# Kernel tuning notes

Measured on AMD Instinct MI355X. Metric: run time of the kernel, lower is better.

The kernel has to match this reference:

```python
import jax, jax.numpy as jnp
import numpy as np
from jax import lax

D_MODEL = 12
D_STATE = 16
D_CONV = 4
D_INNER = 24
DT_RANK = 4
BN_EPS = 1e-5


def _bn(h, gamma, beta, mean, var):
    # inference-mode BatchNorm2d over channel dim (axis=1)
    inv = gamma / jnp.sqrt(var + BN_EPS)
    return h * inv[None, :, None, None] + (beta - mean * inv)[None, :, None, None]


def _mamba(seq, in_proj_w, conv1d_w, conv1d_b, x_proj_w, dt_proj_w, dt_proj_b, A_log, Dp, out_proj_w):
    # seq: (b, L, d_model)
    b, L, _ = seq.shape
    xz = jnp.einsum('bld,ed->ble', seq, in_proj_w)            # (b, L, 2*d_inner)
    u, res = xz[..., :D_INNER], xz[..., D_INNER:]
    # causal depthwise conv1d
    uc = lax.conv_general_dilated(
        u.transpose(0, 2, 1), conv1d_w,                       # (b,d_inner,L), (d_inner,1,d_conv)
        window_strides=(1,), padding=[(D_CONV - 1, 0)],
        feature_group_count=D_INNER,
        dimension_numbers=('NCH', 'OIH', 'NCH'))
    uc = jax.nn.silu((uc + conv1d_b[None, :, None]).transpose(0, 2, 1))  # (b,L,d_inner)
    x_dbl = jnp.einsum('bld,ed->ble', uc, x_proj_w)           # (b,L,dt_rank+2*d_state)
    delta = jax.nn.softplus(
        jnp.einsum('blr,dr->bld', x_dbl[..., :DT_RANK], dt_proj_w) + dt_proj_b)
    Bm = x_dbl[..., DT_RANK:DT_RANK + D_STATE]                # (b,L,n)
    Cm = x_dbl[..., DT_RANK + D_STATE:]                       # (b,L,n)
    A = -jnp.exp(A_log)                                       # (d_inner, n)
    deltaA = jnp.exp(delta[..., None] * A)                    # (b,L,d,n)
    deltaBu = delta[..., None] * Bm[:, :, None, :] * uc[..., None]

    def step(h, inp):
        dA, dBu, c = inp                                      # (b,d,n),(b,d,n),(b,n)
        h = dA * h + dBu
        y = jnp.einsum('bdn,bn->bd', h, c)
        return h, y

    h0 = jnp.zeros((b, D_INNER, D_STATE), seq.dtype)
    _, ys = lax.scan(step, h0, (deltaA.transpose(1, 0, 2, 3),
                                deltaBu.transpose(1, 0, 2, 3),
                                Cm.transpose(1, 0, 2)))
    y = ys.transpose(1, 0, 2) + uc * Dp                       # (b,L,d_inner)
    y = y * jax.nn.silu(res)
    return jnp.einsum('bld,ed->ble', y, out_proj_w)           # (b,L,d_model)


def setup_inputs() -> dict:
    key = jax.random.key(0)
    ks = jax.random.split(key, 16)
    C_IN, C_MID, L = 256, 512, 16384
    d = dict(
        x=jax.random.normal(ks[0], (1, C_IN, L, D_MODEL), jnp.float32),
        conv1_w=jax.random.normal(ks[1], (C_MID, C_IN), jnp.float32) * 0.05,
        conv1_b=jnp.zeros((C_MID,), jnp.float32),
        bn1_gamma=jnp.ones((C_MID,), jnp.float32),
        bn1_beta=jnp.zeros((C_MID,), jnp.float32),
        bn1_mean=jnp.zeros((C_MID,), jnp.float32),
        bn1_var=jnp.ones((C_MID,), jnp.float32),
        conv2_w=jax.random.normal(ks[2], (1, C_MID), jnp.float32) * 0.05,
        conv2_b=jnp.zeros((1,), jnp.float32),
        bn2_gamma=jnp.ones((1,), jnp.float32),
        bn2_beta=jnp.zeros((1,), jnp.float32),
        bn2_mean=jnp.zeros((1,), jnp.float32),
        bn2_var=jnp.ones((1,), jnp.float32),
        in_proj_w=jax.random.normal(ks[3], (2 * D_INNER, D_MODEL), jnp.float32) * 0.2,
        conv1d_w=jax.random.normal(ks[4], (D_INNER, 1, D_CONV), jnp.float32) * 0.3,
        conv1d_b=jnp.zeros((D_INNER,), jnp.float32),
        x_proj_w=jax.random.normal(ks[5], (DT_RANK + 2 * D_STATE, D_INNER), jnp.float32) * 0.2,
        dt_proj_w=jax.random.normal(ks[6], (D_INNER, DT_RANK), jnp.float32) * 0.2,
        dt_proj_b=jax.random.normal(ks[7], (D_INNER,), jnp.float32) * 0.1 - 4.0,
        A_log=jnp.log(jnp.tile(jnp.arange(1, D_STATE + 1, dtype=jnp.float32), (D_INNER, 1))),
        D=jnp.ones((D_INNER,), jnp.float32),
        out_proj_w=jax.random.normal(ks[8], (D_MODEL, D_INNER), jnp.float32) * 0.2,
        lin_w=jax.random.normal(ks[9], (1, D_MODEL), jnp.float32) * 0.3,
        lin_b=jnp.zeros((1,), jnp.float32),
    )
    return d


def reference(x, conv1_w, conv1_b, bn1_gamma, bn1_beta, bn1_mean, bn1_var,
              conv2_w, conv2_b, bn2_gamma, bn2_beta, bn2_mean, bn2_var,
              in_proj_w, conv1d_w, conv1d_b, x_proj_w, dt_proj_w, dt_proj_b,
              A_log, D, out_proj_w, lin_w, lin_b):
    # 1x1 conv stem + BN + ReLU (x2)
    h = jnp.einsum('bchw,oc->bohw', x, conv1_w) + conv1_b[None, :, None, None]
    h = jax.nn.relu(_bn(h, bn1_gamma, bn1_beta, bn1_mean, bn1_var))
    h = jnp.einsum('bchw,oc->bohw', h, conv2_w) + conv2_b[None, :, None, None]
    h = jax.nn.relu(_bn(h, bn2_gamma, bn2_beta, bn2_mean, bn2_var))  # (1,1,L,12)
    seq = h[0]                                                        # squeeze(0) -> (1, L, 12)
    out = _mamba(seq, in_proj_w, conv1d_w, conv1d_b, x_proj_w,
                 dt_proj_w, dt_proj_b, A_log, D, out_proj_w)
    pred = out[:, -1, :] @ lin_w.T + lin_b                            # (1, 1)
    return pred
```

## Files before the change

kernel.cpp:

```cpp
#include <hip/hip_runtime.h>
#include <math.h>

#define L_SEQ 16384
#define DM    12
#define CIN   256
#define CMID  512
#define NPOS  (L_SEQ * DM)
#define DIN   24
#define DST   16

#define OFF_W1T   0u
#define OFF_B1P   131072u
#define OFF_W2P   131584u
#define OFF_MISC  132096u
#define OFF_SEQ   132112u
#define OFF_DELTA 328720u
#define OFF_G     721936u
#define OFF_BW    1115152u
#define OFF_S     1377296u
#define OFF_LAST  1770512u
#define OFF_HL    1770576u
#define WS_FLOATS_NEEDED (OFF_HL + DIN * DST)

__global__ void k0_prep(const float* __restrict__ W1, const float* __restrict__ b1,
                        const float* __restrict__ g1, const float* __restrict__ be1,
                        const float* __restrict__ m1, const float* __restrict__ v1,
                        const float* __restrict__ w2, const float* __restrict__ b2,
                        const float* __restrict__ g2, const float* __restrict__ be2,
                        const float* __restrict__ m2, const float* __restrict__ v2,
                        float* __restrict__ ws) {
    const int o = blockIdx.x;
    const int c = threadIdx.x;
    const float inv1 = g1[o] * rsqrtf(v1[o] + 1e-5f);
    ws[OFF_W1T + (unsigned)c * CMID + o] = W1[o * CIN + c] * inv1;
    if (c == 0) {
        ws[OFF_B1P + o] = b1[o] * inv1 + be1[o] - m1[o] * inv1;
        const float inv2 = g2[0] * rsqrtf(v2[0] + 1e-5f);
        ws[OFF_W2P + o] = w2[o] * inv2;
        if (o == 0) ws[OFF_MISC] = b2[0] * inv2 + be2[0] - m2[0] * inv2;
    }
}

__launch_bounds__(256, 2)
__global__ void k1_gemm(const float* __restrict__ x, const float* __restrict__ wsr,
                        float* __restrict__ seq) {
    __shared__ float Xl[CIN * 64];
    const int tid  = threadIdx.x;
    const int lane = tid & 63;
    const int wv   = __builtin_amdgcn_readfirstlane(tid >> 6);
    const long p0  = (long)blockIdx.x * 64;

    #pragma unroll
    for (int it = 0; it < 16; ++it) {
        const int idx = it * 256 + tid;
        const int row = idx >> 4;
        const int c4  = (idx & 15) << 2;
        *(float4*)&Xl[row * 64 + c4] =
            *(const float4*)&x[(long)row * NPOS + p0 + c4];
    }
    __syncthreads();

    const float* __restrict__ W1T = wsr + OFF_W1T;
    const float* __restrict__ b1p = wsr + OFF_B1P;
    const float* __restrict__ w2p = wsr + OFF_W2P;

    float sp = 0.f;
    for (int ch = 0; ch < 16; ++ch) {
        const int o0 = ch * 32 + wv * 8;
        float acc[8];
        #pragma unroll
        for (int j = 0; j < 8; ++j) acc[j] = 0.f;
        const float* wb = W1T + o0;
        #pragma unroll 4
        for (int c = 0; c < CIN; ++c) {
            const float xv = Xl[c * 64 + lane];
            const float* wr = wb + c * CMID;
            #pragma unroll
            for (int j = 0; j < 8; ++j) acc[j] = fmaf(wr[j], xv, acc[j]);
        }
        #pragma unroll
        for (int j = 0; j < 8; ++j) {
            float h = acc[j] + b1p[o0 + j];
            h = fmaxf(h, 0.f);
            sp = fmaf(w2p[o0 + j], h, sp);
        }
    }

    __syncthreads();
    Xl[wv * 64 + lane] = sp;
    __syncthreads();
    if (wv == 0) {
        const float b2p = wsr[OFF_MISC];
        const float s = Xl[lane] + Xl[64 + lane] + Xl[128 + lane] + Xl[192 + lane];
        seq[p0 + lane] = fmaxf(s + b2p, 0.f);
    }
}

__global__ void k2_front(const float* __restrict__ seq, const float* __restrict__ ipw,
                         const float* __restrict__ cw,  const float* __restrict__ cb,
                         const float* __restrict__ xp,  const float* __restrict__ dtw,
                         const float* __restrict__ dtb, float* __restrict__ ws) {
    const int l = blockIdx.x * 256 + threadIdx.x;

    float srow[4][12];
    #pragma unroll
    for (int k = 0; k < 4; ++k) {
        const int t = l - 3 + k;
        if (t >= 0) {
            #pragma unroll
            for (int q = 0; q < 3; ++q) {
                const float4 v = *(const float4*)&seq[t * 12 + q * 4];
                srow[k][q * 4 + 0] = v.x; srow[k][q * 4 + 1] = v.y;
                srow[k][q * 4 + 2] = v.z; srow[k][q * 4 + 3] = v.w;
            }
        } else {
            #pragma unroll
            for (int m = 0; m < 12; ++m) srow[k][m] = 0.f;
        }
    }

    float uc[DIN];
    #pragma unroll
    for (int d = 0; d < DIN; ++d) {
        float a = cb[d];
        #pragma unroll
        for (int k = 0; k < 4; ++k) {
            float uv = 0.f;
            #pragma unroll
            for (int m = 0; m < 12; ++m) uv = fmaf(srow[k][m], ipw[d * 12 + m], uv);
            a = fmaf(cw[d * 4 + k], uv, a);
        }
        uc[d] = a / (1.f + __expf(-a));
    }

    float dtr[4];
    #pragma unroll
    for (int r = 0; r < 4; ++r) {
        float s = 0.f;
        #pragma unroll
        for (int d = 0; d < DIN; ++d) s = fmaf(uc[d], xp[r * DIN + d], s);
        dtr[r] = s;
    }

    #pragma unroll
    for (int d = 0; d < DIN; ++d) {
        float dp = dtb[d];
        #pragma unroll
        for (int r = 0; r < 4; ++r) dp = fmaf(dtw[d * 4 + r], dtr[r], dp);
        const float de = (dp > 20.f) ? dp : log1pf(__expf(dp));
        ws[OFF_DELTA + (unsigned)d * L_SEQ + l] = de;
        ws[OFF_G     + (unsigned)d * L_SEQ + l] = de * uc[d];
    }

    #pragma unroll
    for (int n = 0; n < DST; ++n) {
        float bv = 0.f;
        #pragma unroll
        for (int d = 0; d < DIN; ++d) bv = fmaf(uc[d], xp[(4 + n) * DIN + d], bv);
        ws[OFF_BW + (unsigned)n * L_SEQ + l] = bv;
    }

    if (l == L_SEQ - 1) {
        #pragma unroll
        for (int d = 0; d < DIN; ++d) ws[OFF_LAST + d] = uc[d];
        #pragma unroll
        for (int n = 0; n < DST; ++n) {
            float cv = 0.f;
            #pragma unroll
            for (int d = 0; d < DIN; ++d) cv = fmaf(uc[d], xp[(20 + n) * DIN + d], cv);
            ws[OFF_LAST + 24 + n] = cv;
        }
        #pragma unroll
        for (int d = 0; d < DIN; ++d) {
            float rv = 0.f;
            #pragma unroll
            for (int m = 0; m < 12; ++m) rv = fmaf(srow[3][m], ipw[(DIN + d) * 12 + m], rv);
            ws[OFF_LAST + 40 + d] = rv;
        }
    }
}

__global__ void k3_scan(const float* __restrict__ delta, float* __restrict__ S) {
    const int d = blockIdx.x;
    const float* dp_ = delta + (size_t)d * L_SEQ;
    float* Sp = S + (size_t)d * L_SEQ;
    const int tid = threadIdx.x;
    __shared__ double part[256];

    double cs = 0.0;
    const int base = tid * 64;
    for (int i = 0; i < 64; ++i) cs += (double)dp_[base + i];
    part[tid] = cs;
    __syncthreads();
    if (tid == 0) {
        double r = 0.0;
        for (int i = 0; i < 256; ++i) { r += part[i]; part[i] = r; }
    }
    __syncthreads();
    const double total = part[255];
    double run = (tid == 0) ? 0.0 : part[tid - 1];
    for (int i = 0; i < 64; ++i) {
        run += (double)dp_[base + i];
        Sp[base + i] = (float)(total - run);
    }
}

__launch_bounds__(256)
__global__ void k4_reduce(const float* __restrict__ A_log, const float* __restrict__ wsr,
                          float* __restrict__ hL) {
    const int d = blockIdx.x;
    const int tid = threadIdx.x;
    float Ar[DST];
    #pragma unroll
    for (int n = 0; n < DST; ++n) Ar[n] = -__expf(A_log[d * DST + n]);

    const float* Sp = wsr + OFF_S + (size_t)d * L_SEQ;
    const float* Gp = wsr + OFF_G + (size_t)d * L_SEQ;
    const float* Bp = wsr + OFF_BW;

    float acc[DST];
    #pragma unroll
    for (int n = 0; n < DST; ++n) acc[n] = 0.f;

    for (int t = tid; t < L_SEQ; t += 256) {
        const float s  = Sp[t];
        const float gv = Gp[t];
        #pragma unroll
        for (int n = 0; n < DST; ++n) {
            const float w = __expf(Ar[n] * s) * gv;
            acc[n] = fmaf(w, Bp[n * L_SEQ + t], acc[n]);
        }
    }

    __shared__ float red[256 * DST];
    #pragma unroll
    for (int n = 0; n < DST; ++n) red[n * 256 + tid] = acc[n];
    __syncthreads();
    for (int st = 128; st >= 1; st >>= 1) {
        if (tid < st) {
            #pragma unroll
            for (int n = 0; n < DST; ++n) red[n * 256 + tid] += red[n * 256 + tid + st];
        }
        __syncthreads();
    }
    if (tid < DST) hL[d * DST + tid] = red[tid * 256];
}

__global__ void k5_final(const float* __restrict__ wsr, const float* __restrict__ Dp,
                         const float* __restrict__ opw, const float* __restrict__ linw,
                         const float* __restrict__ linb, float* __restrict__ out) {
    __shared__ float ybuf[DIN];
    __shared__ float obuf[DM];
    const int tid = threadIdx.x;
    const float* hL   = wsr + OFF_HL;
    const float* last = wsr + OFF_LAST;

    if (tid < DIN) {
        float y = 0.f;
        #pragma unroll
        for (int n = 0; n < DST; ++n) y = fmaf(hL[tid * DST + n], last[24 + n], y);
        y = fmaf(last[tid], Dp[tid], y);
        const float r = last[40 + tid];
        y *= r / (1.f + __expf(-r));
        ybuf[tid] = y;
    }
    __syncthreads();
    if (tid < DM) {
        float o = 0.f;
        #pragma unroll
        for (int dd = 0; dd < DIN; ++dd) o = fmaf(ybuf[dd], opw[tid * DIN + dd], o);
        obuf[tid] = o;
    }
    __syncthreads();
    if (tid == 0) {
        float p = linb[0];
        #pragma unroll
        for (int e = 0; e < DM; ++e) p = fmaf(obuf[e], linw[e], p);
        out[0] = p;
    }
}

__global__ void k_ws_too_small(float* __restrict__ out) {
    if (threadIdx.x == 0 && blockIdx.x == 0) out[0] = -12345.0f;
}

extern "C" void kernel_launch(void* const* d_in, const int* in_sizes, int n_in,
                              void* d_out, int out_size, void* d_ws, size_t ws_size,
                              hipStream_t stream) {
    (void)in_sizes; (void)n_in; (void)out_size;
    float* out = (float*)d_out;
    if (ws_size < (size_t)WS_FLOATS_NEEDED * sizeof(float)) {
        k_ws_too_small<<<dim3(1), dim3(64), 0, stream>>>(out);
        return;
    }

    const float* x    = (const float*)d_in[0];
    const float* w1   = (const float*)d_in[1];
    const float* b1   = (const float*)d_in[2];
    const float* g1   = (const float*)d_in[3];
    const float* be1  = (const float*)d_in[4];
    const float* m1   = (const float*)d_in[5];
    const float* v1   = (const float*)d_in[6];
    const float* w2   = (const float*)d_in[7];
    const float* b2   = (const float*)d_in[8];
    const float* g2   = (const float*)d_in[9];
    const float* be2  = (const float*)d_in[10];
    const float* m2   = (const float*)d_in[11];
    const float* v2   = (const float*)d_in[12];
    const float* ipw  = (const float*)d_in[13];
    const float* cw   = (const float*)d_in[14];
    const float* cb   = (const float*)d_in[15];
    const float* xp   = (const float*)d_in[16];
    const float* dtw  = (const float*)d_in[17];
    const float* dtb  = (const float*)d_in[18];
    const float* alog = (const float*)d_in[19];
    const float* Dp   = (const float*)d_in[20];
    const float* opw  = (const float*)d_in[21];
    const float* linw = (const float*)d_in[22];
    const float* linb = (const float*)d_in[23];

    float* ws = (float*)d_ws;

    k0_prep<<<dim3(CMID), dim3(CIN), 0, stream>>>(w1, b1, g1, be1, m1, v1,
                                                  w2, b2, g2, be2, m2, v2, ws);
    k1_gemm<<<dim3(NPOS / 64), dim3(256), 0, stream>>>(x, ws, ws + OFF_SEQ);
    k2_front<<<dim3(L_SEQ / 256), dim3(256), 0, stream>>>(ws + OFF_SEQ, ipw, cw, cb,
                                                          xp, dtw, dtb, ws);
    k3_scan<<<dim3(DIN), dim3(256), 0, stream>>>(ws + OFF_DELTA, ws + OFF_S);
    k4_reduce<<<dim3(DIN), dim3(256), 0, stream>>>(alog, ws, ws + OFF_HL);
    k5_final<<<dim3(1), dim3(64), 0, stream>>>(ws, Dp, opw, linw, linb, out);
}
```

Measured before the change: 1.980 ms.

## Retile stem GEMM with wider vector weight loads and split scan reduction

The stem GEMM now has each wave own a contiguous 128-channel slab. It processes 16 outputs at a time with float4 weight loads and two input channels per iteration, which cuts scalar load instructions per FMA. The k4 reduction is split into 8 sequence chunks per channel so it runs on 192 blocks instead of 24. k5_final sums the 8 partial results. Other changes: k0_prep is transposed for coalesced writes, k2_front uses 128-thread blocks for more parallelism, and register pressure rises from the 16 accumulators plus 32 loaded weights.

```diff
diff --git a/kernel.cpp b/kernel.cpp
--- a/kernel.cpp
+++ b/kernel.cpp
@@ -20,7 +20,7 @@
 #define OFF_S     1377296u
 #define OFF_LAST  1770512u
 #define OFF_HL    1770576u
-#define WS_FLOATS_NEEDED (OFF_HL + DIN * DST)
+#define WS_FLOATS_NEEDED (OFF_HL + DIN * 8 * DST)
 
 __global__ void k0_prep(const float* __restrict__ W1, const float* __restrict__ b1,
                         const float* __restrict__ g1, const float* __restrict__ be1,
@@ -29,8 +29,8 @@
                         const float* __restrict__ g2, const float* __restrict__ be2,
                         const float* __restrict__ m2, const float* __restrict__ v2,
                         float* __restrict__ ws) {
-    const int o = blockIdx.x;
-    const int c = threadIdx.x;
+    const int c = blockIdx.x;
+    const int o = threadIdx.x;
     const float inv1 = g1[o] * rsqrtf(v1[o] + 1e-5f);
     ws[OFF_W1T + (unsigned)c * CMID + o] = W1[o * CIN + c] * inv1;
     if (c == 0) {
@@ -65,21 +65,32 @@
     const float* __restrict__ w2p = wsr + OFF_W2P;
 
     float sp = 0.f;
-    for (int ch = 0; ch < 16; ++ch) {
-        const int o0 = ch * 32 + wv * 8;
-        float acc[8];
-        #pragma unroll
-        for (int j = 0; j < 8; ++j) acc[j] = 0.f;
-        const float* wb = W1T + o0;
+    #pragma unroll 1
+    for (int ch = 0; ch < 8; ++ch) {
+        const int o0 = __builtin_amdgcn_readfirstlane(wv * 128 + ch * 16);
+        float acc[16];
+        #pragma unroll
+        for (int j = 0; j < 16; ++j) acc[j] = 0.f;
+
         #pragma unroll 4
-        for (int c = 0; c < CIN; ++c) {
-            const float xv = Xl[c * 64 + lane];
-            const float* wr = wb + c * CMID;
-            #pragma unroll
-            for (int j = 0; j < 8; ++j) acc[j] = fmaf(wr[j], xv, acc[j]);
-        }
-        #pragma unroll
-        for (int j = 0; j < 8; ++j) {
+        for (int c = 0; c < CIN; c += 2) {
+            const float xv0 = Xl[c * 64 + lane];
+            const float xv1 = Xl[(c + 1) * 64 + lane];
+            const float4* wq0 = (const float4*)(W1T + (size_t)c * CMID + o0);
+            const float4* wq1 = (const float4*)(W1T + (size_t)(c + 1) * CMID + o0);
+            float w0[16], w1[16];
+            *(float4*)&w0[0]  = wq0[0]; *(float4*)&w0[4]  = wq0[1];
+            *(float4*)&w0[8]  = wq0[2]; *(float4*)&w0[12] = wq0[3];
+            *(float4*)&w1[0]  = wq1[0]; *(float4*)&w1[4]  = wq1[1];
+            *(float4*)&w1[8]  = wq1[2]; *(float4*)&w1[12] = wq1[3];
+            #pragma unroll
+            for (int j = 0; j < 16; ++j) acc[j] = fmaf(w0[j], xv0, acc[j]);
+            #pragma unroll
+            for (int j = 0; j < 16; ++j) acc[j] = fmaf(w1[j], xv1, acc[j]);
+        }
+
+        #pragma unroll
+        for (int j = 0; j < 16; ++j) {
             float h = acc[j] + b1p[o0 + j];
             h = fmaxf(h, 0.f);
             sp = fmaf(w2p[o0 + j], h, sp);
@@ -100,7 +111,7 @@
                          const float* __restrict__ cw,  const float* __restrict__ cb,
                          const float* __restrict__ xp,  const float* __restrict__ dtw,
                          const float* __restrict__ dtb, float* __restrict__ ws) {
-    const int l = blockIdx.x * 256 + threadIdx.x;
+    const int l = blockIdx.x * 128 + threadIdx.x;
 
     float srow[4][12];
     #pragma unroll
@@ -207,9 +218,10 @@
 
 __launch_bounds__(256)
 __global__ void k4_reduce(const float* __restrict__ A_log, const float* __restrict__ wsr,
-                          float* __restrict__ hL) {
-    const int d = blockIdx.x;
-    const int tid = threadIdx.x;
+                          float* __restrict__ part) {
+    const int d     = blockIdx.x >> 3;
+    const int chunk = blockIdx.x & 7;
+    const int tid   = threadIdx.x;
     float Ar[DST];
     #pragma unroll
     for (int n = 0; n < DST; ++n) Ar[n] = -__expf(A_log[d * DST + n]);
@@ -222,7 +234,9 @@
     #pragma unroll
     for (int n = 0; n < DST; ++n) acc[n] = 0.f;
 
-    for (int t = tid; t < L_SEQ; t += 256) {
+    const int t0 = chunk * (L_SEQ / 8);
+    const int t1 = t0 + (L_SEQ / 8);
+    for (int t = t0 + tid; t < t1; t += 256) {
         const float s  = Sp[t];
         const float gv = Gp[t];
         #pragma unroll
@@ -243,7 +257,7 @@
         }
         __syncthreads();
     }
-    if (tid < DST) hL[d * DST + tid] = red[tid * 256];
+    if (tid < DST) part[(size_t)blockIdx.x * DST + tid] = red[tid * 256];
 }
 
 __global__ void k5_final(const float* __restrict__ wsr, const float* __restrict__ Dp,
@@ -252,13 +266,18 @@
     __shared__ float ybuf[DIN];
     __shared__ float obuf[DM];
     const int tid = threadIdx.x;
-    const float* hL   = wsr + OFF_HL;
+    const float* part = wsr + OFF_HL;
     const float* last = wsr + OFF_LAST;
 
     if (tid < DIN) {
         float y = 0.f;
         #pragma unroll
-        for (int n = 0; n < DST; ++n) y = fmaf(hL[tid * DST + n], last[24 + n], y);
+        for (int n = 0; n < DST; ++n) {
+            float h = 0.f;
+            #pragma unroll
+            for (int k = 0; k < 8; ++k) h += part[(size_t)(tid * 8 + k) * DST + n];
+            y = fmaf(h, last[24 + n], y);
+        }
         y = fmaf(last[tid], Dp[tid], y);
         const float r = last[40 + tid];
         y *= r / (1.f + __expf(-r));
@@ -321,12 +340,12 @@
 
     float* ws = (float*)d_ws;
 
-    k0_prep<<<dim3(CMID), dim3(CIN), 0, stream>>>(w1, b1, g1, be1, m1, v1,
+    k0_prep<<<dim3(CIN), dim3(CMID), 0, stream>>>(w1, b1, g1, be1, m1, v1,
                                                   w2, b2, g2, be2, m2, v2, ws);
     k1_gemm<<<dim3(NPOS / 64), dim3(256), 0, stream>>>(x, ws, ws + OFF_SEQ);
-    k2_front<<<dim3(L_SEQ / 256), dim3(256), 0, stream>>>(ws + OFF_SEQ, ipw, cw, cb,
+    k2_front<<<dim3(L_SEQ / 128), dim3(128), 0, stream>>>(ws + OFF_SEQ, ipw, cw, cb,
                                                           xp, dtw, dtb, ws);
     k3_scan<<<dim3(DIN), dim3(256), 0, stream>>>(ws + OFF_DELTA, ws + OFF_S);
-    k4_reduce<<<dim3(DIN), dim3(256), 0, stream>>>(alog, ws, ws + OFF_HL);
+    k4_reduce<<<dim3(DIN * 8), dim3(256), 0, stream>>>(alog, ws, ws + OFF_HL);
     k5_final<<<dim3(1), dim3(64), 0, stream>>>(ws, Dp, opw, linw, linb, out);
 }
```

Measured after the change: 1.595 ms. -19.4%, faster.
